# Kernel tuning notes

Hardware: AMD Instinct MI355X
Metric: run time of the kernel (lower is better)

## Reference

```python
import jax, jax.numpy as jnp
import numpy as np

T = 32400   # bs*H*W BEV queries (1*180*180)
S = 16896   # bs*num_cams*h*w image keys (1*6*32*88)
E = 256     # embed_dim
H = 8       # num_heads
D = 32      # head_dim
MAXL = 32   # max interval length (ref_num_f)


def _mlp(x, w1, b1, w2, b2):
    # nn.Sequential(Linear(E,2E), ReLU, Linear(2E,E))
    return jax.nn.relu(x @ w1 + b1) @ w2 + b2


def setup_inputs() -> dict:
    k0 = jax.random.key(0)
    ks = jax.random.split(k0, 8)
    # ragged interval structure: every BEV cell has an interval of length (idx%32)+1
    lengths = (np.arange(T) % MAXL) + 1
    starts = np.concatenate([np.zeros(1, np.int64), np.cumsum(lengths)[:-1]])
    N = int(lengths.sum())  # 534472 frustum points
    ranks_bev = np.repeat(np.arange(T), lengths)          # sorted by BEV cell
    rng = np.random.default_rng(0)
    ranks_feat = rng.integers(0, S, size=N)               # which key/value row each point reads

    def lin(k, fi, fo):
        return jax.random.normal(k, (fi, fo), jnp.float32) * (1.0 / np.sqrt(fi))

    key_feat = jax.random.normal(ks[1], (S, E), jnp.float32)
    return dict(
        query_depth=jax.random.normal(ks[0], (T, E), jnp.float32),
        key=key_feat,
        value=key_feat,  # module asserts torch.equal(key, value)
        q_w1=lin(ks[2], E, 2 * E), q_b1=jnp.zeros((2 * E,), jnp.float32),
        q_w2=lin(ks[3], 2 * E, E), q_b2=jnp.zeros((E,), jnp.float32),
        k_w1=lin(ks[4], E, 2 * E), k_b1=jnp.zeros((2 * E,), jnp.float32),
        k_w2=lin(ks[5], 2 * E, E), k_b2=jnp.zeros((E,), jnp.float32),
        ranks_feat_f=jnp.asarray(ranks_feat, jnp.int32),
        ranks_bev_f=jnp.asarray(ranks_bev, jnp.int32),
        interval_starts_f=jnp.asarray(starts, jnp.int32),
        interval_lengths_f=jnp.asarray(lengths, jnp.int32),
        ref_num=MAXL,
    )


def reference(query_depth, key, value,
              q_w1, q_b1, q_w2, q_b2,
              k_w1, k_b1, k_w2, k_b2,
              ranks_feat_f, ranks_bev_f,
              interval_starts_f, interval_lengths_f, ref_num):
    scaling = 1.0 / jnp.sqrt(jnp.float32(D))
    q = (_mlp(query_depth, q_w1, q_b1, q_w2, q_b2) * scaling).reshape(T, H, D)
    k = _mlp(key, k_w1, k_b1, k_w2, k_b2).reshape(S, H, D)
    v = value.reshape(S, H, D)

    N = ranks_bev_f.shape[0]
    pt = jnp.arange(N, dtype=jnp.int32)
    # interval id of each point (intervals are contiguous, sorted by start)
    iid = jnp.searchsorted(interval_starts_f, pt, side='right') - 1
    ranks_ref = pt - interval_starts_f[iid]  # within-interval slot, in [0, ref_num)

    # per-point raw attention logit: q[bev] . k[feat] per head  -> [N, H]
    w = jnp.einsum('nhd,nhd->nh', q[ranks_bev_f], k[ranks_feat_f])

    # scatter into ragged weight tensor [T, H, ref_num]; padding masked to -1e9
    attn = jnp.full((T, H, ref_num), -1e9, jnp.float32)
    attn = attn.at[ranks_bev_f, :, ranks_ref].set(w)
    attn = jax.nn.softmax(attn, axis=-1)

    # gather normalized weights back per point and scatter-combine values
    wp = attn[ranks_bev_f, :, ranks_ref]          # [N, H]
    vp = v[ranks_feat_f]                          # [N, H, D]
    out = jnp.zeros((T, H, D), jnp.float32).at[ranks_bev_f].add(wp[:, :, None] * vp)
    return out.reshape(T, E)
```

## Files before the change

### kernel.cpp

```cpp
#include <hip/hip_runtime.h>
#include <hip/hip_bf16.h>
#include <cstdint>
#include <cstddef>

constexpr int T_Q   = 32400;
constexpr int T_PAD = 32512;
constexpr int S_K   = 16896;
constexpr int E_DIM = 256;
constexpr int HID   = 512;

typedef __bf16 bf16x8 __attribute__((ext_vector_type(8)));
typedef float  f32x4  __attribute__((ext_vector_type(4)));
typedef unsigned short ushort8v __attribute__((ext_vector_type(8)));

__device__ __forceinline__ void async16(const __hip_bfloat16* gp, __hip_bfloat16* lp) {
    __builtin_amdgcn_global_load_lds(
        (const __attribute__((address_space(1))) void*)(gp),
        (__attribute__((address_space(3))) void*)(lp), 16, 0, 0);
}

__device__ __forceinline__ float b2f(unsigned short u) {
    return __uint_as_float(((unsigned)u) << 16);
}

constexpr int NB_K = (S_K * E_DIM / 4) / 256;
constexpr int NB_PREP = NB_K + 128;

__global__ __launch_bounds__(256) void prep(
    const float* __restrict__ val_in,
    const float* __restrict__ s0, const float* __restrict__ s1,
    const float* __restrict__ s2, const float* __restrict__ s3,
    __hip_bfloat16* __restrict__ kvB,
    __hip_bfloat16* __restrict__ d0, __hip_bfloat16* __restrict__ d1,
    __hip_bfloat16* __restrict__ d2, __hip_bfloat16* __restrict__ d3) {
    __shared__ float tb[64][65];
    const int b = blockIdx.x;
    const int tid = threadIdx.x;

    if (b < NB_K) {
        int i = (b * 256 + tid) * 4;
        float4 f = *(const float4*)(val_in + i);
        union { ushort4 u4; __hip_bfloat16 bb[4]; } cv;
        cv.bb[0] = __float2bfloat16(f.x);
        cv.bb[1] = __float2bfloat16(f.y);
        cv.bb[2] = __float2bfloat16(f.z);
        cv.bb[3] = __float2bfloat16(f.w);
        int r = i >> 8, c = i & 255;
        *(ushort4*)(kvB + (size_t)r * 512 + 256 + c) = cv.u4;
        return;
    }

    int tloc = b - NB_K;
    int m = tloc >> 5;
    int tt = tloc & 31;
    const float* S = m == 0 ? s0 : m == 1 ? s1 : m == 2 ? s2 : s3;
    __hip_bfloat16* D = m == 0 ? d0 : m == 1 ? d1 : m == 2 ? d2 : d3;
    int Kd, Nd, kt, nt;
    if ((m & 1) == 0) { Kd = 256; Nd = 512; kt = tt & 3; nt = tt >> 2; }
    else              { Kd = 512; Nd = 256; kt = tt & 7; nt = tt >> 3; }
    int tx = tid & 63, ty = tid >> 6;
#pragma unroll
    for (int p = 0; p < 16; ++p) {
        int row = ty * 16 + p;
        tb[row][tx] = S[(size_t)(kt * 64 + row) * Nd + nt * 64 + tx];
    }
    __syncthreads();
#pragma unroll
    for (int p = 0; p < 16; ++p) {
        int row = ty * 16 + p;
        D[(size_t)(nt * 64 + row) * Kd + kt * 64 + tx] = __float2bfloat16(tb[tx][row]);
    }
}


__global__ __launch_bounds__(256) void gemm1(
    const float* __restrict__ Aq, const float* __restrict__ Ak,
    const __hip_bfloat16* __restrict__ BTq, const __hip_bfloat16* __restrict__ BTk,
    const float* __restrict__ biasq, const float* __restrict__ biask,
    __hip_bfloat16* __restrict__ Cq, __hip_bfloat16* __restrict__ Ck,
    int qtiles) {
    __shared__ __hip_bfloat16 As[64 * 64];
    __shared__ __hip_bfloat16 Bs[256 * 64];

    const int tm = blockIdx.x >> 1;
    const int tn = blockIdx.x & 1;
    const bool isq = tm < qtiles;
    const float* A  = isq ? Aq : Ak;
    const __hip_bfloat16* BT = isq ? BTq : BTk;
    const float* bias = isq ? biasq : biask;
    __hip_bfloat16* C = isq ? Cq : Ck;
    const int mrow0 = (isq ? tm : tm - qtiles) * 64;
    const int rowlim = isq ? T_Q : S_K;
    const int n0 = tn * 256;

    const int tid = threadIdx.x;
    const int w = tid >> 6, l = tid & 63;
    const int lm = l & 15, lq = l >> 4;
    const int wn = w * 64;
    const int srow8 = l >> 3;
    const int u8 = l & 7;
    const int pu8 = u8 ^ srow8;
    const int scolB = (u8 ^ srow8) << 3;

    f32x4 acc[4][4] = {};

    for (int k0 = 0; k0 < 256; k0 += 64) {
#pragma unroll
        for (int c = 0; c < 2; ++c) {
            int r = w * 16 + c * 8 + srow8;
            int gr = mrow0 + r;
            float4 f0 = make_float4(0.f, 0.f, 0.f, 0.f);
            float4 f1 = make_float4(0.f, 0.f, 0.f, 0.f);
            if (gr < rowlim) {
                const float* ap = A + (size_t)gr * 256 + k0 + u8 * 8;
                f0 = *(const float4*)ap;
                f1 = *(const float4*)(ap + 4);
            }
            union { bf16x8 v; __hip_bfloat16 b[8]; } cv;
            cv.b[0] = __float2bfloat16(f0.x); cv.b[1] = __float2bfloat16(f0.y);
            cv.b[2] = __float2bfloat16(f0.z); cv.b[3] = __float2bfloat16(f0.w);
            cv.b[4] = __float2bfloat16(f1.x); cv.b[5] = __float2bfloat16(f1.y);
            cv.b[6] = __float2bfloat16(f1.z); cv.b[7] = __float2bfloat16(f1.w);
            *(bf16x8*)(As + r * 64 + pu8 * 8) = cv.v;
        }
#pragma unroll
        for (int c = 0; c < 8; ++c) {
            int r = w * 64 + c * 8 + srow8;
            async16(BT + (size_t)(n0 + r) * 256 + k0 + scolB,
                    Bs + (w * 64 + c * 8) * 64);
        }
        __syncthreads();

#pragma unroll
        for (int ks = 0; ks < 2; ++ks) {
            bf16x8 af[4], bfr[4];
#pragma unroll
            for (int mi = 0; mi < 4; ++mi) {
                int row = mi * 16 + lm;
                int pu = (ks * 4 + lq) ^ (row & 7);
                af[mi] = *(const bf16x8*)(As + row * 64 + pu * 8);
            }
#pragma unroll
            for (int ni = 0; ni < 4; ++ni) {
                int row = wn + ni * 16 + lm;
                int pu = (ks * 4 + lq) ^ (row & 7);
                bfr[ni] = *(const bf16x8*)(Bs + row * 64 + pu * 8);
            }
#pragma unroll
            for (int mi = 0; mi < 4; ++mi)
#pragma unroll
                for (int ni = 0; ni < 4; ++ni)
                    acc[mi][ni] = __builtin_amdgcn_mfma_f32_16x16x32_bf16(
                        af[mi], bfr[ni], acc[mi][ni], 0, 0, 0);
        }
        __syncthreads();
    }

#pragma unroll
    for (int ni = 0; ni < 4; ++ni) {
        int col = n0 + wn + ni * 16 + lm;
        float bv = bias[col];
#pragma unroll
        for (int mi = 0; mi < 4; ++mi) {
            size_t rowb = (size_t)mrow0 + mi * 16 + lq * 4;
#pragma unroll
            for (int r = 0; r < 4; ++r) {
                float vv = fmaxf(acc[mi][ni][r] + bv, 0.f);
                C[(rowb + r) * HID + col] = __float2bfloat16(vv);
            }
        }
    }
}

__global__ __launch_bounds__(256) void gemm2(
    const __hip_bfloat16* __restrict__ Aq, const __hip_bfloat16* __restrict__ Ak,
    const __hip_bfloat16* __restrict__ BTq, const __hip_bfloat16* __restrict__ BTk,
    const float* __restrict__ biasq, const float* __restrict__ biask,
    __hip_bfloat16* __restrict__ Cq, __hip_bfloat16* __restrict__ Ck,
    float scaleq, int qtiles) {
    __shared__ __hip_bfloat16 As[64 * 64];
    __shared__ __hip_bfloat16 Bs[256 * 64];

    const int tm = blockIdx.x;
    const bool isq = tm < qtiles;
    const __hip_bfloat16* A  = isq ? Aq : Ak;
    const __hip_bfloat16* BT = isq ? BTq : BTk;
    const float* bias = isq ? biasq : biask;
    __hip_bfloat16* C = isq ? Cq : Ck;
    const int ldc = isq ? E_DIM : 512;
    const float scale = isq ? scaleq : 1.0f;
    const int mrow0 = (isq ? tm : tm - qtiles) * 64;

    const int tid = threadIdx.x;
    const int w = tid >> 6, l = tid & 63;
    const int lm = l & 15, lq = l >> 4;
    const int wn = w * 64;
    const int srow8 = l >> 3;
    const int u8 = l & 7;
    const int scol = (u8 ^ srow8) << 3;

    f32x4 acc[4][4] = {};

    for (int k0 = 0; k0 < 512; k0 += 64) {
#pragma unroll
        for (int c = 0; c < 2; ++c) {
            int r = w * 16 + c * 8 + srow8;
            async16(A + (size_t)(mrow0 + r) * 512 + k0 + scol,
                    As + (w * 16 + c * 8) * 64);
        }
#pragma unroll
        for (int c = 0; c < 8; ++c) {
            int r = w * 64 + c * 8 + srow8;
            async16(BT + (size_t)r * 512 + k0 + scol,
                    Bs + (w * 64 + c * 8) * 64);
        }
        __syncthreads();

#pragma unroll
        for (int ks = 0; ks < 2; ++ks) {
            bf16x8 af[4], bfr[4];
#pragma unroll
            for (int mi = 0; mi < 4; ++mi) {
                int row = mi * 16 + lm;
                int pu = (ks * 4 + lq) ^ (row & 7);
                af[mi] = *(const bf16x8*)(As + row * 64 + pu * 8);
            }
#pragma unroll
            for (int ni = 0; ni < 4; ++ni) {
                int row = wn + ni * 16 + lm;
                int pu = (ks * 4 + lq) ^ (row & 7);
                bfr[ni] = *(const bf16x8*)(Bs + row * 64 + pu * 8);
            }
#pragma unroll
            for (int mi = 0; mi < 4; ++mi)
#pragma unroll
                for (int ni = 0; ni < 4; ++ni)
                    acc[mi][ni] = __builtin_amdgcn_mfma_f32_16x16x32_bf16(
                        af[mi], bfr[ni], acc[mi][ni], 0, 0, 0);
        }
        __syncthreads();
    }

#pragma unroll
    for (int ni = 0; ni < 4; ++ni) {
        int col = wn + ni * 16 + lm;
        float bv = bias[col];
#pragma unroll
        for (int mi = 0; mi < 4; ++mi) {
            size_t rowb = (size_t)mrow0 + mi * 16 + lq * 4;
#pragma unroll
            for (int r = 0; r < 4; ++r) {
                float vv = (acc[mi][ni][r] + bv) * scale;
                C[(rowb + r) * ldc + col] = __float2bfloat16(vv);
            }
        }
    }
}

#define PREF1(BUF, C)                                                        \
    {                                                                        \
        int f_ = __shfl(myf, (C));                                           \
        BUF = *(const ushort8v*)(kv + ((size_t)f_ << 9) + (l << 3));         \
    }

#define PROC1(BUF)                                                           \
    {                                                                        \
        float wv = 0.f;                                                      \
        _Pragma("unroll") for (int i = 0; i < 8; ++i)                        \
            wv = fmaf(qf[i], b2f(BUF[i]), wv);                               \
        wv += __shfl_xor(wv, 1);                                             \
        wv += __shfl_xor(wv, 2);                                             \
        float t2 = __shfl_xor(wv, 32);                                       \
        float sc = half ? t2 : wv;                                           \
        float mn = fmaxf(m, sc);                                             \
        float al = __expf(m - mn);                                           \
        float p  = __expf(sc - mn);                                          \
        m = mn;                                                              \
        s = fmaf(s, al, p);                                                  \
        _Pragma("unroll") for (int i = 0; i < 8; ++i)                        \
            a[i] = fmaf(p, b2f(BUF[i]), a[i] * al);                          \
    }

#define STEP(BUF, J)                                                         \
    if (c + (J) < L) {                                                       \
        PROC1(BUF);                                                          \
        if (c + (J) + 6 < L) PREF1(BUF, c + (J) + 6);                        \
    }

__global__ __launch_bounds__(256) void attn_kernel(
    const __hip_bfloat16* __restrict__ q,
    const __hip_bfloat16* __restrict__ kv,
    const int* __restrict__ rf,
    const int* __restrict__ starts,
    const int* __restrict__ lens,
    float* __restrict__ out) {
    int t = blockIdx.x * 4 + (threadIdx.x >> 6);
    if (t >= T_Q) return;
    int l = threadIdx.x & 63;
    int half = l >> 5, sub = l & 31;
    int su = __builtin_amdgcn_readfirstlane(starts[t]);
    int L  = __builtin_amdgcn_readfirstlane(lens[t]);

    int li = l < L - 1 ? l : L - 1;
    int myf = rf[su + li];

    ushort8v qu = *(const ushort8v*)(q + (size_t)t * 256 + sub * 8);
    float qf[8];
#pragma unroll
    for (int i = 0; i < 8; ++i) qf[i] = b2f(qu[i]);

    float m = -INFINITY, s = 0.f;
    float a[8] = {0.f, 0.f, 0.f, 0.f, 0.f, 0.f, 0.f, 0.f};

    ushort8v b0 = {}, b1 = {}, b2 = {}, b3 = {}, b4 = {}, b5 = {};
    PREF1(b0, 0);
    if (L > 1) PREF1(b1, 1);
    if (L > 2) PREF1(b2, 2);
    if (L > 3) PREF1(b3, 3);
    if (L > 4) PREF1(b4, 4);
    if (L > 5) PREF1(b5, 5);

    for (int c = 0; c < L; c += 6) {
        STEP(b0, 0)
        STEP(b1, 1)
        STEP(b2, 2)
        STEP(b3, 3)
        STEP(b4, 4)
        STEP(b5, 5)
    }

    if (half) {
        float inv = 1.f / s;
        float* op = out + (size_t)t * 256 + sub * 8;
        float4 o0, o1;
        o0.x = a[0] * inv; o0.y = a[1] * inv; o0.z = a[2] * inv; o0.w = a[3] * inv;
        o1.x = a[4] * inv; o1.y = a[5] * inv; o1.z = a[6] * inv; o1.w = a[7] * inv;
        *(float4*)op = o0;
        *(float4*)(op + 4) = o1;
    }
}

extern "C" void kernel_launch(void* const* d_in, const int* in_sizes, int n_in,
                              void* d_out, int out_size, void* d_ws, size_t ws_size,
                              hipStream_t stream) {
    const float* q_in   = (const float*)d_in[0];
    const float* key_in = (const float*)d_in[1];
    const float* val_in = (const float*)d_in[2];
    const float* q_w1   = (const float*)d_in[3];
    const float* q_b1   = (const float*)d_in[4];
    const float* q_w2   = (const float*)d_in[5];
    const float* q_b2   = (const float*)d_in[6];
    const float* k_w1   = (const float*)d_in[7];
    const float* k_b1   = (const float*)d_in[8];
    const float* k_w2   = (const float*)d_in[9];
    const float* k_b2   = (const float*)d_in[10];
    const int* ranks_feat = (const int*)d_in[11];
    const int* starts     = (const int*)d_in[13];
    const int* lens       = (const int*)d_in[14];
    float* out = (float*)d_out;

    char* ws = (char*)d_ws;
    size_t off = 0;
    auto alloc = [&](size_t bytes) {
        char* p = ws + off;
        off += (bytes + 255) & ~(size_t)255;
        return p;
    };
    __hip_bfloat16* hidQ = (__hip_bfloat16*)alloc((size_t)T_PAD * HID * 2);
    __hip_bfloat16* hidK = (__hip_bfloat16*)alloc((size_t)S_K * HID * 2);
    __hip_bfloat16* qMl  = (__hip_bfloat16*)alloc((size_t)T_PAD * E_DIM * 2);
    __hip_bfloat16* kvB  = (__hip_bfloat16*)alloc((size_t)S_K * 512 * 2);
    __hip_bfloat16* w1qT = (__hip_bfloat16*)alloc((size_t)HID * E_DIM * 2);
    __hip_bfloat16* w2qT = (__hip_bfloat16*)alloc((size_t)E_DIM * HID * 2);
    __hip_bfloat16* w1kT = (__hip_bfloat16*)alloc((size_t)HID * E_DIM * 2);
    __hip_bfloat16* w2kT = (__hip_bfloat16*)alloc((size_t)E_DIM * HID * 2);
    (void)ws_size; (void)n_in; (void)out_size; (void)in_sizes;

    prep<<<NB_PREP, 256, 0, stream>>>(val_in, q_w1, q_w2, k_w1, k_w2,
                                      kvB, w1qT, w2qT, w1kT, w2kT);

    const float qscale = 0.17677669529663687f;
    const int QT = T_PAD / 64;
    const int KT = S_K / 64;

    gemm1<<<(QT + KT) * 2, 256, 0, stream>>>(
        q_in, key_in, w1qT, w1kT, q_b1, k_b1, hidQ, hidK, QT);
    gemm2<<<QT + KT, 256, 0, stream>>>(
        hidQ, hidK, w2qT, w2kT, q_b2, k_b2, qMl, kvB, qscale, QT);

    attn_kernel<<<T_Q / 4, 256, 0, stream>>>(qMl, kvB, ranks_feat, starts, lens, out);
}
```

Baseline: 292.8 us.

## Process two keys per wavefront with half-wave split and lazy softmax rescale

The attention kernel now assigns each half of a wavefront its own key (even/odd slot), so each lane loads separate K and V halves and a wavefront handles two keys per step instead of one, halving the serial loop length. Online softmax skips the rescale when no lane sees a new maximum (wave-uniform check). The partial sums are merged across the two halves at the end. The launch becomes a grid-stride persistent loop over a fixed number of blocks. Risks are extra cross-lane shuffles, divergence on the rescale branch, and tail imbalance from the fixed grid.

```diff
diff --git a/kernel.cpp b/kernel.cpp
--- a/kernel.cpp
+++ b/kernel.cpp
@@ -257,35 +257,48 @@
     }
 }
 
-#define PREF1(BUF, C)                                                        \
+
+#define PREFP(KB, VB, C)                                                     \
     {                                                                        \
-        int f_ = __shfl(myf, (C));                                           \
-        BUF = *(const ushort8v*)(kv + ((size_t)f_ << 9) + (l << 3));         \
-    }
-
-#define PROC1(BUF)                                                           \
+        int f_ = __shfl(myf, (C) + half);                                    \
+        const __hip_bfloat16* p_ = kv + ((size_t)f_ << 9) + (sub << 3);      \
+        KB = *(const ushort8v*)p_;                                           \
+        VB = *(const ushort8v*)(p_ + 256);                                   \
+    }
+
+#define PROCP(KB, VB, C)                                                     \
     {                                                                        \
         float wv = 0.f;                                                      \
         _Pragma("unroll") for (int i = 0; i < 8; ++i)                        \
-            wv = fmaf(qf[i], b2f(BUF[i]), wv);                               \
+            wv = fmaf(qf[i], b2f(KB[i]), wv);                                \
         wv += __shfl_xor(wv, 1);                                             \
         wv += __shfl_xor(wv, 2);                                             \
-        float t2 = __shfl_xor(wv, 32);                                       \
-        float sc = half ? t2 : wv;                                           \
-        float mn = fmaxf(m, sc);                                             \
-        float al = __expf(m - mn);                                           \
-        float p  = __expf(sc - mn);                                          \
-        m = mn;                                                              \
-        s = fmaf(s, al, p);                                                  \
-        _Pragma("unroll") for (int i = 0; i < 8; ++i)                        \
-            a[i] = fmaf(p, b2f(BUF[i]), a[i] * al);                          \
-    }
-
-#define STEP(BUF, J)                                                         \
+        float sc = ((C) + half < L) ? wv : -1e30f;                           \
+        float so = __shfl_xor(sc, 32);                                       \
+        float pm = fmaxf(sc, so);                                            \
+        if (__all(pm <= m)) {                                                \
+            float p = __expf(sc - m);                                        \
+            s += p;                                                          \
+            _Pragma("unroll") for (int i = 0; i < 8; ++i)                    \
+                a[i] = fmaf(p, b2f(VB[i]), a[i]);                            \
+        } else {                                                             \
+            float mn = fmaxf(m, pm);                                         \
+            float al = __expf(m - mn);                                       \
+            float p  = __expf(sc - mn);                                      \
+            m = mn;                                                          \
+            s = fmaf(s, al, p);                                              \
+            _Pragma("unroll") for (int i = 0; i < 8; ++i)                    \
+                a[i] = fmaf(p, b2f(VB[i]), a[i] * al);                       \
+        }                                                                    \
+    }
+
+#define STEPP(KB, VB, J)                                                     \
     if (c + (J) < L) {                                                       \
-        PROC1(BUF);                                                          \
-        if (c + (J) + 6 < L) PREF1(BUF, c + (J) + 6);                        \
-    }
+        PROCP(KB, VB, c + (J));                                              \
+        if (c + (J) + 6 < L) PREFP(KB, VB, c + (J) + 6);                     \
+    }
+
+constexpr int ATTN_BLOCKS = 2026;
 
 __global__ __launch_bounds__(256) void attn_kernel(
     const __hip_bfloat16* __restrict__ q,
@@ -294,49 +307,50 @@
     const int* __restrict__ starts,
     const int* __restrict__ lens,
     float* __restrict__ out) {
-    int t = blockIdx.x * 4 + (threadIdx.x >> 6);
-    if (t >= T_Q) return;
-    int l = threadIdx.x & 63;
-    int half = l >> 5, sub = l & 31;
-    int su = __builtin_amdgcn_readfirstlane(starts[t]);
-    int L  = __builtin_amdgcn_readfirstlane(lens[t]);
-
-    int li = l < L - 1 ? l : L - 1;
-    int myf = rf[su + li];
-
-    ushort8v qu = *(const ushort8v*)(q + (size_t)t * 256 + sub * 8);
-    float qf[8];
-#pragma unroll
-    for (int i = 0; i < 8; ++i) qf[i] = b2f(qu[i]);
-
-    float m = -INFINITY, s = 0.f;
-    float a[8] = {0.f, 0.f, 0.f, 0.f, 0.f, 0.f, 0.f, 0.f};
-
-    ushort8v b0 = {}, b1 = {}, b2 = {}, b3 = {}, b4 = {}, b5 = {};
-    PREF1(b0, 0);
-    if (L > 1) PREF1(b1, 1);
-    if (L > 2) PREF1(b2, 2);
-    if (L > 3) PREF1(b3, 3);
-    if (L > 4) PREF1(b4, 4);
-    if (L > 5) PREF1(b5, 5);
-
-    for (int c = 0; c < L; c += 6) {
-        STEP(b0, 0)
-        STEP(b1, 1)
-        STEP(b2, 2)
-        STEP(b3, 3)
-        STEP(b4, 4)
-        STEP(b5, 5)
-    }
-
-    if (half) {
-        float inv = 1.f / s;
-        float* op = out + (size_t)t * 256 + sub * 8;
-        float4 o0, o1;
-        o0.x = a[0] * inv; o0.y = a[1] * inv; o0.z = a[2] * inv; o0.w = a[3] * inv;
-        o1.x = a[4] * inv; o1.y = a[5] * inv; o1.z = a[6] * inv; o1.w = a[7] * inv;
-        *(float4*)op = o0;
-        *(float4*)(op + 4) = o1;
+    const int wid = threadIdx.x >> 6;
+    const int l = threadIdx.x & 63;
+    const int sub = l & 31, half = l >> 5;
+    const int tstride = gridDim.x * 4;
+
+    for (int t = blockIdx.x * 4 + wid; t < T_Q; t += tstride) {
+        int su = __builtin_amdgcn_readfirstlane(starts[t]);
+        int L  = __builtin_amdgcn_readfirstlane(lens[t]);
+
+        int li = l < L - 1 ? l : L - 1;
+        int myf = rf[su + li];
+
+        ushort8v qu = *(const ushort8v*)(q + (size_t)t * 256 + sub * 8);
+        float qf[8];
+#pragma unroll
+        for (int i = 0; i < 8; ++i) qf[i] = b2f(qu[i]);
+
+        float m = -INFINITY, s = 0.f;
+        float a[8] = {0.f, 0.f, 0.f, 0.f, 0.f, 0.f, 0.f, 0.f};
+
+        ushort8v k0 = {}, v0 = {}, k1 = {}, v1 = {}, k2 = {}, v2 = {};
+        PREFP(k0, v0, 0);
+        if (L > 2) PREFP(k1, v1, 2);
+        if (L > 4) PREFP(k2, v2, 4);
+
+        for (int c = 0; c < L; c += 6) {
+            STEPP(k0, v0, 0)
+            STEPP(k1, v1, 2)
+            STEPP(k2, v2, 4)
+        }
+
+        float st = s + __shfl_xor(s, 32);
+#pragma unroll
+        for (int i = 0; i < 8; ++i) a[i] += __shfl_xor(a[i], 32);
+
+        if (half) {
+            float inv = 1.f / st;
+            float* op = out + (size_t)t * 256 + sub * 8;
+            float4 o0, o1;
+            o0.x = a[0] * inv; o0.y = a[1] * inv; o0.z = a[2] * inv; o0.w = a[3] * inv;
+            o1.x = a[4] * inv; o1.y = a[5] * inv; o1.z = a[6] * inv; o1.w = a[7] * inv;
+            *(float4*)op = o0;
+            *(float4*)(op + 4) = o1;
+        }
     }
 }
 
@@ -388,5 +402,5 @@
     gemm2<<<QT + KT, 256, 0, stream>>>(
         hidQ, hidK, w2qT, w2kT, q_b2, k_b2, qMl, kvB, qscale, QT);
 
-    attn_kernel<<<T_Q / 4, 256, 0, stream>>>(qMl, kvB, ranks_feat, starts, lens, out);
-}
+    attn_kernel<<<ATTN_BLOCKS, 256, 0, stream>>>(qMl, kvB, ranks_feat, starts, lens, out);
+}
```

After: 269.4 us. 8.0% less time.
